# Optimization experiments

Measured on AMD Instinct MI355X. Metric: run time of the kernel, lower is better.

## Reference

```python
import jax, jax.numpy as jnp
import numpy as np

T = 8          # num_timesteps
H = 8          # num_heads
D = 128        # lifting_dim
ROPE_BASE = 10000.0


def apply_time_only_rope(x, num_nodes, num_timesteps, base=ROPE_BASE):
    # x: [B, H, num_nodes*num_timesteps, d_head], time-major flattening
    B, Hh, S, dh = x.shape
    half = dh // 2
    times = jnp.arange(num_timesteps, dtype=jnp.float32)
    freqs = 1.0 / base ** (2.0 * jnp.arange(half, dtype=jnp.float32) / dh)
    angle = times[:, None] * freqs[None, :]                 # [T, half]
    positions = jnp.repeat(jnp.arange(num_timesteps), num_nodes)  # [S]
    cos_g = jnp.cos(angle)[positions]                       # [S, half]
    sin_g = jnp.sin(angle)[positions]
    t1 = x[..., 0::2]
    t2 = x[..., 1::2]
    r0 = t1 * cos_g - t2 * sin_g
    r1 = t1 * sin_g + t2 * cos_g
    return jnp.stack([r0, r1], axis=-1).reshape(x.shape)


def setup_inputs() -> dict:
    key = jax.random.key(0)
    ks = jax.random.split(key, 16)
    B_T, N, E = 32, 2048, 8192
    inp = {
        'x_0': jax.random.normal(ks[0], (B_T, N, D), jnp.float32),
        'edge_attr': jax.random.normal(ks[1], (B_T, E, D), jnp.float32),
        'q_data': jax.random.normal(ks[2], (B_T, N, D), jnp.float32),
    }
    def lin(k):
        kw, kb = jax.random.split(k)
        return (jax.random.normal(kw, (D, D), jnp.float32) * 0.02,
                jax.random.normal(kb, (D,), jnp.float32) * 0.02)
    inp['Wq'], inp['bq'] = lin(ks[3])
    inp['Wk0'], inp['bk0'] = lin(ks[4])
    inp['Wv0'], inp['bv0'] = lin(ks[5])
    inp['Wk1'], inp['bk1'] = lin(ks[6])
    inp['Wv1'], inp['bv1'] = lin(ks[7])
    inp['Wo'], inp['bo'] = lin(ks[8])
    return inp


def reference(x_0, edge_attr, q_data, Wq, bq, Wk0, bk0, Wv0, bv0, Wk1, bk1, Wv1, bv1, Wo, bo):
    B_T, N, d = x_0.shape
    B = B_T // T
    dh = d // H

    def flatten_st(a):  # [B*T, M, d] -> [B, T*M, d]
        return a.reshape(B, T * a.shape[1], d)

    qf = flatten_st(q_data) @ Wq.T + bq                     # [B, T*N, d]
    q = qf.reshape(B, H, N * T, dh)                         # faithful torch .view
    q = jax.nn.softmax(q, axis=-1)
    q = apply_time_only_rope(q, N, T)

    out = q
    for (feat, Wk, bk, Wv, bv) in ((x_0, Wk0, bk0, Wv0, bv0),
                                   (edge_attr, Wk1, bk1, Wv1, bv1)):
        M = feat.shape[1]
        hf = flatten_st(feat)                               # [B, T*M, d]
        k = (hf @ Wk.T + bk).reshape(B, H, M * T, dh)
        v = (hf @ Wv.T + bv).reshape(B, H, M * T, dh)
        k = apply_time_only_rope(k, M, T)
        k = jax.nn.softmax(k, axis=-1)
        k_cumsum = k.sum(axis=-2, keepdims=True)            # [B,H,1,dh]
        D_inv = 1.0 / jnp.maximum((q * k_cumsum).sum(axis=-1, keepdims=True), 1e-8)
        kv = jnp.einsum('bhsd,bhse->bhde', k, v)            # [B,H,dh,dh]
        out = q + jnp.einsum('bhsd,bhde->bhse', q, kv) * D_inv

    out = out.transpose(0, 2, 1, 3).reshape(B, N * T, d)
    out = out @ Wo.T + bo
    return out.reshape(B * T, N, d)                         # unflatten_spatiotemporal
```

## Files before the change

kernel.cpp:

```cpp
#include <hip/hip_runtime.h>
#include <hip/hip_bf16.h>
#include <math.h>


typedef __attribute__((ext_vector_type(8))) short short8;
typedef __attribute__((ext_vector_type(4))) float float4v;

#define LN1E4_OVER8 1.1512925464970229f

#define OFF_QWS   0
#define OFF_FRG_Q 4194304
#define OFF_FRG_O 4202496
#define OFF_BFRG  4210688
#define OFF_KV    4227072
#define OFF_KCS   4235264
#define OFF_PART  4235776

__device__ __forceinline__ unsigned short f2bf(float f) {
    __hip_bfloat16 h = __float2bfloat16(f);
    return *reinterpret_cast<unsigned short*>(&h);
}
__device__ __forceinline__ float bf2f(unsigned short s) {
    return __uint_as_float(((unsigned)s) << 16);
}
__device__ __forceinline__ unsigned pk2(float a, float b) {
    __hip_bfloat162 h = __float22bfloat162_rn(make_float2(a, b));
    return *reinterpret_cast<unsigned*>(&h);
}
template<int C> __device__ __forceinline__ float dppadd(float x) {
    int r = __builtin_amdgcn_update_dpp(0, __float_as_int(x), C, 0xF, 0xF, true);
    return x + __int_as_float(r);
}
__device__ __forceinline__ float sum16(float x) {
    x = dppadd<0xB1>(x);
    x = dppadd<0x4E>(x);
    x = dppadd<0x141>(x);
    x = dppadd<0x140>(x);
    return x;
}
__device__ __forceinline__ float qperm1(float x) {
    int r = __builtin_amdgcn_update_dpp(0, __float_as_int(x), 0xB1, 0xF, 0xF, true);
    return __int_as_float(r);
}

__global__ void k_prep(const float* __restrict__ Wq, const float* __restrict__ Wk1,
                       const float* __restrict__ Wv1, const float* __restrict__ Wo,
                       float* __restrict__ ws) {
    int i = blockIdx.x * 256 + threadIdx.x;
    if (i < 32768) {
        int j = i & 16383;
        int jE = j & 7, lane = (j >> 3) & 63, km = (j >> 9) & 3, cg = j >> 11;
        int n = cg * 16 + (lane & 15);
        int kk = km * 32 + (lane >> 4) * 8 + jE;
        const float* W = (i < 16384) ? Wq : Wo;
        unsigned short* dst = (unsigned short*)(ws + ((i < 16384) ? OFF_FRG_Q : OFF_FRG_O));
        dst[j] = f2bf(W[n * 128 + kk]);
    } else if (i < 65536) {
        int j = i - 32768;
        int jE = j & 7, lane = (j >> 3) & 63, km = (j >> 9) & 3, cg = j >> 11;
        int n = cg * 16 + (lane & 15);
        int k = km * 32 + (lane >> 4) * 8 + jE;
        float w = (cg < 8) ? Wk1[n * 128 + k] : Wv1[(n - 128) * 128 + k];
        ((unsigned short*)(ws + OFF_BFRG))[j] = f2bf(w);
    } else {
        int j = i - 65536;
        if (j < 8704) ws[OFF_KV + j] = 0.f;
    }
}

__global__ __launch_bounds__(256, 4) void k_q(const float* __restrict__ qd,
                                              const float* __restrict__ bq,
                                              float* __restrict__ ws) {
    __shared__ __align__(16) unsigned short aT[128 * 128];
    unsigned* qws32 = (unsigned*)(ws + OFF_QWS);
    int t = threadIdx.x, blk = blockIdx.x;
    int wave = t >> 6, lane = t & 63, quad = lane >> 4, n = lane & 15;
    long base = (long)blk * 128;
    int b = blk >> 7;
    int h = (blk & 127) >> 4;
    int s0 = (blk & 15) * 1024;
    int t1 = (blk & 15) >> 1;

    const short8* fq = (const short8*)((const unsigned short*)(ws + OFF_FRG_Q));
    short8 Bf[2][4];
    #pragma unroll
    for (int ct = 0; ct < 2; ++ct)
        #pragma unroll
        for (int km = 0; km < 4; ++km)
            Bf[ct][km] = fq[((2 * wave + ct) * 4 + km) * 64 + lane];

    #pragma unroll
    for (int i = 0; i < 16; ++i) {
        int idx = i * 256 + t;
        int row = idx >> 5, c4 = idx & 31;
        float4 v = ((const float4*)qd)[(base + row) * 32 + c4];
        unsigned short* p = aT + row * 128 + (((c4 >> 1) ^ (row & 7)) << 3) + (c4 & 1) * 4;
        *(uint2*)p = make_uint2(pk2(v.x, v.y), pk2(v.z, v.w));
    }
    __syncthreads();

    float fr = __expf(-LN1E4_OVER8 * (float)(n >> 1));
    float sa, ca; __sincosf((float)t1 * fr, &sa, &ca);
    float sgn = (n & 1) ? sa : -sa;
    float bias0 = bq[(2 * wave) * 16 + n];
    float bias1 = bq[(2 * wave + 1) * 16 + n];

    #pragma unroll
    for (int rt = 0; rt < 8; ++rt) {
        float4v a0 = (float4v){0.f, 0.f, 0.f, 0.f};
        float4v a1 = (float4v){0.f, 0.f, 0.f, 0.f};
        int row = rt * 16 + n;
        #pragma unroll
        for (int km = 0; km < 4; ++km) {
            short8 Af = *(const short8*)(aT + row * 128 + (((km * 4 + quad) ^ (n & 7)) << 3));
            a0 = __builtin_amdgcn_mfma_f32_16x16x32_bf16(Af, Bf[0][km], a0, 0, 0, 0);
            a1 = __builtin_amdgcn_mfma_f32_16x16x32_bf16(Af, Bf[1][km], a1, 0, 0, 0);
        }
        #pragma unroll
        for (int ct = 0; ct < 2; ++ct) {
            int cg = 2 * wave + ct;
            float bias = ct ? bias1 : bias0;
            float4v x = ct ? a1 : a0;
            #pragma unroll
            for (int i = 0; i < 4; ++i) {
                float e = __expf(x[i] + bias);
                float s = sum16(e);
                float q = e / s;
                float r = fmaf(qperm1(q), sgn, q * ca);
                unsigned pkd = ((unsigned)f2bf(qperm1(r)) << 16) | (unsigned)f2bf(r);
                if ((n & 1) == 0) {
                    int sp = s0 + (rt * 16 + quad * 4 + i) * 8 + cg;
                    long qoff = ((long)(b * 8 + h) * 16384 + sp) * 16 + n;
                    qws32[qoff >> 1] = pkd;
                }
            }
        }
    }
}

__global__ __launch_bounds__(256, 4) void k_kv(const float* __restrict__ ea,
                                               const float* __restrict__ bk,
                                               const float* __restrict__ bv,
                                               float* __restrict__ ws) {
    __shared__ __align__(16) char smem[40960];
    unsigned short* aT = (unsigned short*)smem;

    int t = threadIdx.x, blk = blockIdx.x;
    int wave = t >> 6, lane = t & 63, quad = lane >> 4, n = lane & 15;
    unsigned short* kbuf = (unsigned short*)(smem + 32768) + wave * 1024;
    unsigned short* vbuf = kbuf + 512;
    long base = (long)blk * 128;
    int sl = (blk & 511) << 7;
    int t2 = (sl & 8191) >> 10;

    #pragma unroll
    for (int i = 0; i < 16; ++i) {
        int idx = i * 256 + t;
        int row = idx >> 5, c4 = idx & 31;
        float4 v = ((const float4*)ea)[(base + row) * 32 + c4];
        unsigned short* p = aT + row * 128 + (((c4 >> 1) ^ (row & 7)) << 3) + (c4 & 1) * 4;
        *(uint2*)p = make_uint2(pk2(v.x, v.y), pk2(v.z, v.w));
    }

    const short8* bfrag = (const short8*)((const unsigned short*)(ws + OFF_BFRG));
    short8 Bf[4][4];
    #pragma unroll
    for (int ct = 0; ct < 4; ++ct) {
        int cg = (ct < 2) ? (2 * wave + ct) : (8 + 2 * wave + (ct - 2));
        #pragma unroll
        for (int km = 0; km < 4; ++km)
            Bf[ct][km] = bfrag[(cg * 4 + km) * 64 + lane];
    }

    float bias[4];
    #pragma unroll
    for (int ct = 0; ct < 4; ++ct)
        bias[ct] = (ct < 2) ? bk[(2 * wave + ct) * 16 + n] : bv[(2 * wave + ct - 2) * 16 + n];
    float fr = __expf(-LN1E4_OVER8 * (float)(n >> 1));
    float sv, cvv; __sincosf((float)t2 * fr, &sv, &cvv);
    float sgn = (n & 1) ? sv : -sv;
    float kcsacc = 0.f;
    float4v kvacc = (float4v){0.f, 0.f, 0.f, 0.f};

    __syncthreads();

    #pragma unroll
    for (int rt = 0; rt < 8; ++rt) {
        float4v acc[4];
        #pragma unroll
        for (int ct = 0; ct < 4; ++ct) acc[ct] = (float4v){0.f, 0.f, 0.f, 0.f};

        int row = rt * 16 + n;
        short8 Af[4];
        #pragma unroll
        for (int km = 0; km < 4; ++km)
            Af[km] = *(const short8*)(aT + row * 128 + (((km * 4 + quad) ^ (n & 7)) << 3));
        __builtin_amdgcn_s_setprio(1);
        #pragma unroll
        for (int ct = 0; ct < 4; ++ct)
            #pragma unroll
            for (int km = 0; km < 4; ++km)
                acc[ct] = __builtin_amdgcn_mfma_f32_16x16x32_bf16(Af[km], Bf[ct][km], acc[ct], 0, 0, 0);
        __builtin_amdgcn_s_setprio(0);

        #pragma unroll
        for (int ct = 0; ct < 4; ++ct) {
            float x0 = acc[ct][0] + bias[ct];
            float x1 = acc[ct][1] + bias[ct];
            float x2 = acc[ct][2] + bias[ct];
            float x3 = acc[ct][3] + bias[ct];
            if (ct < 2) {
                x0 = fmaf(qperm1(x0), sgn, x0 * cvv); x1 = fmaf(qperm1(x1), sgn, x1 * cvv);
                x2 = fmaf(qperm1(x2), sgn, x2 * cvv); x3 = fmaf(qperm1(x3), sgn, x3 * cvv);
                x0 = __expf(x0); x1 = __expf(x1); x2 = __expf(x2); x3 = __expf(x3);
                float s0 = sum16(x0), s1 = sum16(x1), s2 = sum16(x2), s3 = sum16(x3);
                x0 /= s0; x1 /= s1; x2 /= s2; x3 /= s3;
                kcsacc += x0 + x1 + x2 + x3;
            }
            unsigned short* dst = (ct < 2) ? kbuf : vbuf;
            int o = (ct & 1) * 16 + quad * 4;
            *(uint2*)(dst + n * 32 + (((o >> 3) ^ (n & 3)) << 3) + (o & 7)) =
                make_uint2(pk2(x0, x1), pk2(x2, x3));
        }

        asm volatile("s_waitcnt lgkmcnt(0)" ::: "memory");
        __builtin_amdgcn_sched_barrier(0);

        {
            int off = ((quad ^ (n & 3)) << 3);
            short8 Ak = *(const short8*)(kbuf + n * 32 + off);
            short8 Bv = *(const short8*)(vbuf + n * 32 + off);
            kvacc = __builtin_amdgcn_mfma_f32_16x16x32_bf16(Ak, Bv, kvacc, 0, 0, 0);
        }
    }

    kcsacc += __shfl_xor(kcsacc, 16); kcsacc += __shfl_xor(kcsacc, 32);
    float* part = ws + OFF_PART + ((long)blk * 4 + wave) * 272;
    #pragma unroll
    for (int r = 0; r < 4; ++r) part[(quad * 4 + r) * 16 + n] = kvacc[r];
    if (lane < 16) part[256 + n] = kcsacc;
}

__global__ void k_red(float* __restrict__ ws) {
    int blk = blockIdx.x, t = threadIdx.x;
    if (t >= 272) return;
    int bh = blk >> 3, g = blk & 7;
    const float* part = ws + OFF_PART + (long)bh * 256 * 272 + (long)g * 32 * 272 + t;
    float s = 0.f;
    #pragma unroll 8
    for (int i = 0; i < 32; ++i) s += part[(long)i * 272];
    float* dst = (t < 256) ? (ws + OFF_KV + bh * 256 + t)
                           : (ws + OFF_KCS + bh * 16 + (t - 256));
    atomicAdd(dst, s);
}

__global__ __launch_bounds__(256, 3) void k_out(const float* __restrict__ bo,
                                                float* __restrict__ ws,
                                                float* __restrict__ out) {
    __shared__ __align__(16) unsigned short tile[128 * 128];
    const unsigned short* qws16 = (const unsigned short*)(ws + OFF_QWS);
    int t = threadIdx.x, blk = blockIdx.x;
    int wave = t >> 6, lane = t & 63, quad = lane >> 4, n = lane & 15;
    int b = blk >> 7;
    int sp0 = (blk & 127) * 128;

    #pragma unroll
    for (int i = 0; i < 16; ++i) {
        int idx = i * 256 + t;
        int h = idx >> 9, rr = (idx >> 2) & 127, seg = idx & 3;
        uint2 u = *(const uint2*)(qws16 + ((long)(b * 8 + h) * 16384 + sp0 + rr) * 16 + seg * 4);
        unsigned short* p = tile + rr * 128 + (((h * 2 + (seg >> 1)) ^ (rr & 7)) << 3) + (seg & 1) * 4;
        *(uint2*)p = u;
    }

    short8 Bkv[2], Bden[2];
    #pragma unroll
    for (int ct = 0; ct < 2; ++ct) {
        int h = 2 * wave + ct;
        const float* kvp = ws + OFF_KV + (b * 8 + h) * 256;
        const float* ksp = ws + OFF_KCS + (b * 8 + h) * 16;
        short8 bk8 = {0, 0, 0, 0, 0, 0, 0, 0}, bd8 = {0, 0, 0, 0, 0, 0, 0, 0};
        bool act = (ct == 0) ? (quad < 2) : (quad >= 2);
        int kbase = (ct == 0) ? quad * 8 : (quad - 2) * 8;
        if (act) {
            #pragma unroll
            for (int jj = 0; jj < 8; ++jj) {
                bk8[jj] = (short)f2bf(kvp[(kbase + jj) * 16 + n]);
                bd8[jj] = (short)f2bf(ksp[kbase + jj]);
            }
        }
        Bkv[ct] = bk8; Bden[ct] = bd8;
    }
    const short8* fo = (const short8*)((const unsigned short*)(ws + OFF_FRG_O));
    short8 Bo[2][4];
    #pragma unroll
    for (int ct = 0; ct < 2; ++ct)
        #pragma unroll
        for (int km = 0; km < 4; ++km)
            Bo[ct][km] = fo[((2 * wave + ct) * 4 + km) * 64 + lane];
    __syncthreads();

    #pragma unroll
    for (int pass = 0; pass < 2; ++pass) {
        unsigned short fh[4][2][4];
        #pragma unroll
        for (int rtl = 0; rtl < 4; ++rtl) {
            int rt = pass * 4 + rtl;
            int row = rt * 16 + n;
            short8 Af = *(const short8*)(tile + row * 128 + (((wave * 4 + quad) ^ (n & 7)) << 3));
            float4v P0 = __builtin_amdgcn_mfma_f32_16x16x32_bf16(Af, Bkv[0], (float4v){0.f,0.f,0.f,0.f}, 0, 0, 0);
            float4v P1 = __builtin_amdgcn_mfma_f32_16x16x32_bf16(Af, Bkv[1], (float4v){0.f,0.f,0.f,0.f}, 0, 0, 0);
            float4v D0 = __builtin_amdgcn_mfma_f32_16x16x32_bf16(Af, Bden[0], (float4v){0.f,0.f,0.f,0.f}, 0, 0, 0);
            float4v D1 = __builtin_amdgcn_mfma_f32_16x16x32_bf16(Af, Bden[1], (float4v){0.f,0.f,0.f,0.f}, 0, 0, 0);
            #pragma unroll
            for (int ct = 0; ct < 2; ++ct) {
                int cg = 2 * wave + ct;
                float4v P = ct ? P1 : P0;
                float4v D = ct ? D1 : D0;
                #pragma unroll
                for (int i = 0; i < 4; ++i) {
                    int rw = rt * 16 + quad * 4 + i;
                    int col = cg * 16 + n;
                    float qv = bf2f(tile[rw * 128 + (((col >> 3) ^ (rw & 7)) << 3) + (col & 7)]);
                    float inv = 1.0f / fmaxf(D[i], 1e-8f);
                    fh[rtl][ct][i] = f2bf(fmaf(P[i], inv, qv));
                }
            }
        }
        __syncthreads();
        #pragma unroll
        for (int rtl = 0; rtl < 4; ++rtl)
            #pragma unroll
            for (int ct = 0; ct < 2; ++ct) {
                int cg = 2 * wave + ct;
                #pragma unroll
                for (int i = 0; i < 4; ++i) {
                    int rw = (pass * 4 + rtl) * 16 + quad * 4 + i;
                    int col = cg * 16 + n;
                    tile[rw * 128 + (((col >> 3) ^ (rw & 7)) << 3) + (col & 7)] = fh[rtl][ct][i];
                }
            }
    }
    __syncthreads();

    float bb0 = bo[(2 * wave) * 16 + n];
    float bb1 = bo[(2 * wave + 1) * 16 + n];
    #pragma unroll
    for (int rt = 0; rt < 8; ++rt) {
        float4v a0 = (float4v){0.f, 0.f, 0.f, 0.f};
        float4v a1 = (float4v){0.f, 0.f, 0.f, 0.f};
        int row = rt * 16 + n;
        #pragma unroll
        for (int km = 0; km < 4; ++km) {
            short8 Af = *(const short8*)(tile + row * 128 + (((km * 4 + quad) ^ (n & 7)) << 3));
            a0 = __builtin_amdgcn_mfma_f32_16x16x32_bf16(Af, Bo[0][km], a0, 0, 0, 0);
            a1 = __builtin_amdgcn_mfma_f32_16x16x32_bf16(Af, Bo[1][km], a1, 0, 0, 0);
        }
        #pragma unroll
        for (int ct = 0; ct < 2; ++ct) {
            int cg = 2 * wave + ct;
            float bb = ct ? bb1 : bb0;
            float4v a = ct ? a1 : a0;
            #pragma unroll
            for (int i = 0; i < 4; ++i) {
                float v = a[i] + bb;
                float pv = qperm1(v);
                if ((n & 1) == 0) {
                    long rg = (long)b * 16384 + sp0 + rt * 16 + quad * 4 + i;
                    *(float2*)(out + rg * 128 + cg * 16 + n) = make_float2(v, pv);
                }
            }
        }
    }
}

extern "C" void kernel_launch(void* const* d_in, const int* in_sizes, int n_in,
                              void* d_out, int out_size, void* d_ws, size_t ws_size,
                              hipStream_t stream) {
    (void)in_sizes; (void)n_in; (void)out_size; (void)ws_size;
    const float* edge = (const float*)d_in[1];
    const float* qd   = (const float*)d_in[2];
    const float* Wq   = (const float*)d_in[3];
    const float* bq   = (const float*)d_in[4];
    const float* Wk1  = (const float*)d_in[9];
    const float* bk1  = (const float*)d_in[10];
    const float* Wv1  = (const float*)d_in[11];
    const float* bv1  = (const float*)d_in[12];
    const float* Wo   = (const float*)d_in[13];
    const float* bo   = (const float*)d_in[14];
    float* ws  = (float*)d_ws;
    float* out = (float*)d_out;

    hipLaunchKernelGGL(k_prep, dim3(290),  dim3(256), 0, stream, Wq, Wk1, Wv1, Wo, ws);
    hipLaunchKernelGGL(k_q,    dim3(512),  dim3(256), 0, stream, qd, bq, ws);
    hipLaunchKernelGGL(k_kv,   dim3(2048), dim3(256), 0, stream, edge, bk1, bv1, ws);
    hipLaunchKernelGGL(k_red,  dim3(256),  dim3(320), 0, stream, ws);
    hipLaunchKernelGGL(k_out,  dim3(512),  dim3(256), 0, stream, bo, ws, out);
}
```

Before: 298.9 us.

## Merge Q and KV kernels into one interleaved launch, halve k_out tile

Fuses the Q-projection kernel and the KV-projection kernel into one launch of 2560 blocks, where every fifth block does the Q work and the rest do KV work. This removes a launch boundary and lets the two independent stages overlap on the GPU. It also swaps IEEE divisions for hardware reciprocal approximations in the softmax and normalisation, and adds setprio around the Q MFMAs. k_out now uses 64-row tiles with twice the blocks and 4 waves-per-EU occupancy.

```diff
diff --git a/kernel.cpp b/kernel.cpp
--- a/kernel.cpp
+++ b/kernel.cpp
@@ -26,6 +26,9 @@
 __device__ __forceinline__ unsigned pk2(float a, float b) {
     __hip_bfloat162 h = __float22bfloat162_rn(make_float2(a, b));
     return *reinterpret_cast<unsigned*>(&h);
+}
+__device__ __forceinline__ float frcp(float x) {
+    return __builtin_amdgcn_rcpf(x);
 }
 template<int C> __device__ __forceinline__ float dppadd(float x) {
     int r = __builtin_amdgcn_update_dpp(0, __float_as_int(x), C, 0xF, 0xF, true);
@@ -68,85 +71,88 @@
     }
 }
 
-__global__ __launch_bounds__(256, 4) void k_q(const float* __restrict__ qd,
-                                              const float* __restrict__ bq,
-                                              float* __restrict__ ws) {
-    __shared__ __align__(16) unsigned short aT[128 * 128];
-    unsigned* qws32 = (unsigned*)(ws + OFF_QWS);
-    int t = threadIdx.x, blk = blockIdx.x;
+__global__ __launch_bounds__(256, 4) void k_main(const float* __restrict__ ea,
+                                                 const float* __restrict__ bk,
+                                                 const float* __restrict__ bv,
+                                                 const float* __restrict__ qd,
+                                                 const float* __restrict__ bq,
+                                                 float* __restrict__ ws) {
+    __shared__ __align__(16) char smem[40960];
+    int t = threadIdx.x;
     int wave = t >> 6, lane = t & 63, quad = lane >> 4, n = lane & 15;
-    long base = (long)blk * 128;
-    int b = blk >> 7;
-    int h = (blk & 127) >> 4;
-    int s0 = (blk & 15) * 1024;
-    int t1 = (blk & 15) >> 1;
-
-    const short8* fq = (const short8*)((const unsigned short*)(ws + OFF_FRG_Q));
-    short8 Bf[2][4];
-    #pragma unroll
-    for (int ct = 0; ct < 2; ++ct)
-        #pragma unroll
-        for (int km = 0; km < 4; ++km)
-            Bf[ct][km] = fq[((2 * wave + ct) * 4 + km) * 64 + lane];
-
-    #pragma unroll
-    for (int i = 0; i < 16; ++i) {
-        int idx = i * 256 + t;
-        int row = idx >> 5, c4 = idx & 31;
-        float4 v = ((const float4*)qd)[(base + row) * 32 + c4];
-        unsigned short* p = aT + row * 128 + (((c4 >> 1) ^ (row & 7)) << 3) + (c4 & 1) * 4;
-        *(uint2*)p = make_uint2(pk2(v.x, v.y), pk2(v.z, v.w));
-    }
-    __syncthreads();
-
-    float fr = __expf(-LN1E4_OVER8 * (float)(n >> 1));
-    float sa, ca; __sincosf((float)t1 * fr, &sa, &ca);
-    float sgn = (n & 1) ? sa : -sa;
-    float bias0 = bq[(2 * wave) * 16 + n];
-    float bias1 = bq[(2 * wave + 1) * 16 + n];
-
-    #pragma unroll
-    for (int rt = 0; rt < 8; ++rt) {
-        float4v a0 = (float4v){0.f, 0.f, 0.f, 0.f};
-        float4v a1 = (float4v){0.f, 0.f, 0.f, 0.f};
-        int row = rt * 16 + n;
-        #pragma unroll
-        for (int km = 0; km < 4; ++km) {
-            short8 Af = *(const short8*)(aT + row * 128 + (((km * 4 + quad) ^ (n & 7)) << 3));
-            a0 = __builtin_amdgcn_mfma_f32_16x16x32_bf16(Af, Bf[0][km], a0, 0, 0, 0);
-            a1 = __builtin_amdgcn_mfma_f32_16x16x32_bf16(Af, Bf[1][km], a1, 0, 0, 0);
-        }
-        #pragma unroll
-        for (int ct = 0; ct < 2; ++ct) {
-            int cg = 2 * wave + ct;
-            float bias = ct ? bias1 : bias0;
-            float4v x = ct ? a1 : a0;
-            #pragma unroll
-            for (int i = 0; i < 4; ++i) {
-                float e = __expf(x[i] + bias);
-                float s = sum16(e);
-                float q = e / s;
-                float r = fmaf(qperm1(q), sgn, q * ca);
-                unsigned pkd = ((unsigned)f2bf(qperm1(r)) << 16) | (unsigned)f2bf(r);
-                if ((n & 1) == 0) {
-                    int sp = s0 + (rt * 16 + quad * 4 + i) * 8 + cg;
-                    long qoff = ((long)(b * 8 + h) * 16384 + sp) * 16 + n;
-                    qws32[qoff >> 1] = pkd;
+    int g = blockIdx.x;
+
+    if (g % 5 == 4) {
+        int blk = g / 5;
+        unsigned short* aT = (unsigned short*)smem;
+        unsigned* qws32 = (unsigned*)(ws + OFF_QWS);
+        long base = (long)blk * 128;
+        int b = blk >> 7;
+        int h = (blk & 127) >> 4;
+        int s0 = (blk & 15) * 1024;
+        int t1 = (blk & 15) >> 1;
+
+        const short8* fq = (const short8*)((const unsigned short*)(ws + OFF_FRG_Q));
+        short8 Bf[2][4];
+        #pragma unroll
+        for (int ct = 0; ct < 2; ++ct)
+            #pragma unroll
+            for (int km = 0; km < 4; ++km)
+                Bf[ct][km] = fq[((2 * wave + ct) * 4 + km) * 64 + lane];
+
+        #pragma unroll
+        for (int i = 0; i < 16; ++i) {
+            int idx = i * 256 + t;
+            int row = idx >> 5, c4 = idx & 31;
+            float4 v = ((const float4*)qd)[(base + row) * 32 + c4];
+            unsigned short* p = aT + row * 128 + (((c4 >> 1) ^ (row & 7)) << 3) + (c4 & 1) * 4;
+            *(uint2*)p = make_uint2(pk2(v.x, v.y), pk2(v.z, v.w));
+        }
+        __syncthreads();
+
+        float fr = __expf(-LN1E4_OVER8 * (float)(n >> 1));
+        float sa, ca; __sincosf((float)t1 * fr, &sa, &ca);
+        float sgn = (n & 1) ? sa : -sa;
+        float bias0 = bq[(2 * wave) * 16 + n];
+        float bias1 = bq[(2 * wave + 1) * 16 + n];
+
+        #pragma unroll
+        for (int rt = 0; rt < 8; ++rt) {
+            float4v a0 = (float4v){0.f, 0.f, 0.f, 0.f};
+            float4v a1 = (float4v){0.f, 0.f, 0.f, 0.f};
+            int row = rt * 16 + n;
+            __builtin_amdgcn_s_setprio(1);
+            #pragma unroll
+            for (int km = 0; km < 4; ++km) {
+                short8 Af = *(const short8*)(aT + row * 128 + (((km * 4 + quad) ^ (n & 7)) << 3));
+                a0 = __builtin_amdgcn_mfma_f32_16x16x32_bf16(Af, Bf[0][km], a0, 0, 0, 0);
+                a1 = __builtin_amdgcn_mfma_f32_16x16x32_bf16(Af, Bf[1][km], a1, 0, 0, 0);
+            }
+            __builtin_amdgcn_s_setprio(0);
+            #pragma unroll
+            for (int ct = 0; ct < 2; ++ct) {
+                int cg = 2 * wave + ct;
+                float bias = ct ? bias1 : bias0;
+                float4v x = ct ? a1 : a0;
+                #pragma unroll
+                for (int i = 0; i < 4; ++i) {
+                    float e = __expf(x[i] + bias);
+                    float q = e * frcp(sum16(e));
+                    float r = fmaf(qperm1(q), sgn, q * ca);
+                    unsigned pkd = ((unsigned)f2bf(qperm1(r)) << 16) | (unsigned)f2bf(r);
+                    if ((n & 1) == 0) {
+                        int sp = s0 + (rt * 16 + quad * 4 + i) * 8 + cg;
+                        long qoff = ((long)(b * 8 + h) * 16384 + sp) * 16 + n;
+                        qws32[qoff >> 1] = pkd;
+                    }
                 }
             }
         }
-    }
-}
-
-__global__ __launch_bounds__(256, 4) void k_kv(const float* __restrict__ ea,
-                                               const float* __restrict__ bk,
-                                               const float* __restrict__ bv,
-                                               float* __restrict__ ws) {
-    __shared__ __align__(16) char smem[40960];
+        return;
+    }
+
+    int blk = g - g / 5;
     unsigned short* aT = (unsigned short*)smem;
-
-    int t = threadIdx.x, blk = blockIdx.x;
-    int wave = t >> 6, lane = t & 63, quad = lane >> 4, n = lane & 15;
     unsigned short* kbuf = (unsigned short*)(smem + 32768) + wave * 1024;
     unsigned short* vbuf = kbuf + 512;
     long base = (long)blk * 128;
@@ -213,8 +219,8 @@
                 x0 = fmaf(qperm1(x0), sgn, x0 * cvv); x1 = fmaf(qperm1(x1), sgn, x1 * cvv);
                 x2 = fmaf(qperm1(x2), sgn, x2 * cvv); x3 = fmaf(qperm1(x3), sgn, x3 * cvv);
                 x0 = __expf(x0); x1 = __expf(x1); x2 = __expf(x2); x3 = __expf(x3);
-                float s0 = sum16(x0), s1 = sum16(x1), s2 = sum16(x2), s3 = sum16(x3);
-                x0 /= s0; x1 /= s1; x2 /= s2; x3 /= s3;
+                x0 *= frcp(sum16(x0)); x1 *= frcp(sum16(x1));
+                x2 *= frcp(sum16(x2)); x3 *= frcp(sum16(x3));
                 kcsacc += x0 + x1 + x2 + x3;
             }
             unsigned short* dst = (ct < 2) ? kbuf : vbuf;
@@ -254,20 +260,20 @@
     atomicAdd(dst, s);
 }
 
-__global__ __launch_bounds__(256, 3) void k_out(const float* __restrict__ bo,
+__global__ __launch_bounds__(256, 4) void k_out(const float* __restrict__ bo,
                                                 float* __restrict__ ws,
                                                 float* __restrict__ out) {
-    __shared__ __align__(16) unsigned short tile[128 * 128];
+    __shared__ __align__(16) unsigned short tile[64 * 128];
     const unsigned short* qws16 = (const unsigned short*)(ws + OFF_QWS);
     int t = threadIdx.x, blk = blockIdx.x;
     int wave = t >> 6, lane = t & 63, quad = lane >> 4, n = lane & 15;
-    int b = blk >> 7;
-    int sp0 = (blk & 127) * 128;
-
-    #pragma unroll
-    for (int i = 0; i < 16; ++i) {
+    int b = blk >> 8;
+    int sp0 = (blk & 255) * 64;
+
+    #pragma unroll
+    for (int i = 0; i < 8; ++i) {
         int idx = i * 256 + t;
-        int h = idx >> 9, rr = (idx >> 2) & 127, seg = idx & 3;
+        int h = idx >> 8, rr = (idx >> 2) & 63, seg = idx & 3;
         uint2 u = *(const uint2*)(qws16 + ((long)(b * 8 + h) * 16384 + sp0 + rr) * 16 + seg * 4);
         unsigned short* p = tile + rr * 128 + (((h * 2 + (seg >> 1)) ^ (rr & 7)) << 3) + (seg & 1) * 4;
         *(uint2*)p = u;
@@ -302,10 +308,10 @@
 
     #pragma unroll
     for (int pass = 0; pass < 2; ++pass) {
-        unsigned short fh[4][2][4];
-        #pragma unroll
-        for (int rtl = 0; rtl < 4; ++rtl) {
-            int rt = pass * 4 + rtl;
+        unsigned short fh[2][2][4];
+        #pragma unroll
+        for (int rtl = 0; rtl < 2; ++rtl) {
+            int rt = pass * 2 + rtl;
             int row = rt * 16 + n;
             short8 Af = *(const short8*)(tile + row * 128 + (((wave * 4 + quad) ^ (n & 7)) << 3));
             float4v P0 = __builtin_amdgcn_mfma_f32_16x16x32_bf16(Af, Bkv[0], (float4v){0.f,0.f,0.f,0.f}, 0, 0, 0);
@@ -322,20 +328,20 @@
                     int rw = rt * 16 + quad * 4 + i;
                     int col = cg * 16 + n;
                     float qv = bf2f(tile[rw * 128 + (((col >> 3) ^ (rw & 7)) << 3) + (col & 7)]);
-                    float inv = 1.0f / fmaxf(D[i], 1e-8f);
+                    float inv = frcp(fmaxf(D[i], 1e-8f));
                     fh[rtl][ct][i] = f2bf(fmaf(P[i], inv, qv));
                 }
             }
         }
         __syncthreads();
         #pragma unroll
-        for (int rtl = 0; rtl < 4; ++rtl)
+        for (int rtl = 0; rtl < 2; ++rtl)
             #pragma unroll
             for (int ct = 0; ct < 2; ++ct) {
                 int cg = 2 * wave + ct;
                 #pragma unroll
                 for (int i = 0; i < 4; ++i) {
-                    int rw = (pass * 4 + rtl) * 16 + quad * 4 + i;
+                    int rw = (pass * 2 + rtl) * 16 + quad * 4 + i;
                     int col = cg * 16 + n;
                     tile[rw * 128 + (((col >> 3) ^ (rw & 7)) << 3) + (col & 7)] = fh[rtl][ct][i];
                 }
@@ -346,7 +352,7 @@
     float bb0 = bo[(2 * wave) * 16 + n];
     float bb1 = bo[(2 * wave + 1) * 16 + n];
     #pragma unroll
-    for (int rt = 0; rt < 8; ++rt) {
+    for (int rt = 0; rt < 4; ++rt) {
         float4v a0 = (float4v){0.f, 0.f, 0.f, 0.f};
         float4v a1 = (float4v){0.f, 0.f, 0.f, 0.f};
         int row = rt * 16 + n;
@@ -392,8 +398,7 @@
     float* out = (float*)d_out;
 
     hipLaunchKernelGGL(k_prep, dim3(290),  dim3(256), 0, stream, Wq, Wk1, Wv1, Wo, ws);
-    hipLaunchKernelGGL(k_q,    dim3(512),  dim3(256), 0, stream, qd, bq, ws);
-    hipLaunchKernelGGL(k_kv,   dim3(2048), dim3(256), 0, stream, edge, bk1, bv1, ws);
+    hipLaunchKernelGGL(k_main, dim3(2560), dim3(256), 0, stream, edge, bk1, bv1, qd, bq, ws);
     hipLaunchKernelGGL(k_red,  dim3(256),  dim3(320), 0, stream, ws);
-    hipLaunchKernelGGL(k_out,  dim3(512),  dim3(256), 0, stream, bo, ws, out);
-}
+    hipLaunchKernelGGL(k_out,  dim3(1024), dim3(256), 0, stream, bo, ws, out);
+}
```

New measurement: 283.0 us. -5.3%, faster.
